# Kernel tuning notes

Measured on AMD Instinct MI355X. Metric: run time of the kernel, lower is better.

Reference implementation:

```python
import jax, jax.numpy as jnp
import numpy as np
import math

EMBED_SIZE = 2048
HEADS = 32
GROUPS = 8
HEAD_DIM = EMBED_SIZE // HEADS          # 64
HPG = HEADS // GROUPS                   # heads per group = 4
N, L = 4, 1024


def setup_inputs() -> dict:
    key = jax.random.key(0)
    k1, k2, k3, k4, k5 = jax.random.split(key, 5)
    values = jax.random.normal(k1, (N, L, EMBED_SIZE), dtype=jnp.float32)
    keys = jax.random.normal(k2, (N, L, EMBED_SIZE), dtype=jnp.float32)
    queries = jax.random.normal(k3, (N, L, EMBED_SIZE), dtype=jnp.float32)
    mask = jnp.ones((N, 1, 1, L, L), dtype=jnp.int32)
    # fc_out: Linear(heads*head_dim -> embed_size), torch default init ~ U(-1/sqrt(in), 1/sqrt(in))
    bound = 1.0 / math.sqrt(EMBED_SIZE)
    W_out = jax.random.uniform(k4, (EMBED_SIZE, EMBED_SIZE), jnp.float32, -bound, bound)
    b_out = jax.random.uniform(k5, (EMBED_SIZE,), jnp.float32, -bound, bound)
    return {"values": values, "keys": keys, "queries": queries, "mask": mask,
            "W_out": W_out, "b_out": b_out}


def reference(values, keys, queries, mask, W_out, b_out):
    n, q_len, _ = queries.shape
    k_len = keys.shape[1]
    # split into (N, L, groups, heads_per_group, head_dim)
    v = values.reshape(n, k_len, GROUPS, HPG, HEAD_DIM)
    k = keys.reshape(n, k_len, GROUPS, HPG, HEAD_DIM)
    q = queries.reshape(n, q_len, GROUPS, HPG, HEAD_DIM)
    # scores: (N, groups, heads_per_group, q, k)
    energy = jnp.einsum('nqghd,nkghd->nghqk', q, k)
    energy = jnp.where(mask == 0, jnp.float32(-1e20), energy)
    attn = jax.nn.softmax(energy / jnp.sqrt(jnp.float32(EMBED_SIZE)), axis=-1)
    out = jnp.einsum('nghqk,nkghd->nqghd', attn, v).reshape(n, q_len, EMBED_SIZE)
    return out @ W_out.T + b_out
```

## Files before the change

kernel.cpp:

```cpp
#include <hip/hip_runtime.h>
#include <math.h>


#define LSEQ 1024
#define EMB  2048

typedef __bf16 bf16x8 __attribute__((ext_vector_type(8)));
typedef __bf16 bf16x4 __attribute__((ext_vector_type(4)));
typedef float floatx4 __attribute__((ext_vector_type(4)));
typedef unsigned short ushort8v __attribute__((ext_vector_type(8)));

__device__ __forceinline__ float4 ld4(const float* p) { return *(const float4*)p; }

__device__ __forceinline__ unsigned short f2bf(float x) {
    unsigned u = __float_as_uint(x);
    u += 0x7FFFu + ((u >> 16) & 1u);
    return (unsigned short)(u >> 16);
}

__device__ __forceinline__ void gl_lds16(const void* g, void* l) {
    __builtin_amdgcn_global_load_lds((const __attribute__((address_space(1))) void*)g,
                                     (__attribute__((address_space(3))) void*)l, 16, 0, 0);
}

__device__ __forceinline__ void stage64(const unsigned short* g, size_t gstride,
                                        unsigned short* lds) {
    const int t = threadIdx.x;
    #pragma unroll
    for (int h = 0; h < 2; h++) {
        const int idx = h * 256 + t;
        const int r   = idx >> 3;
        const int sl  = (idx & 7) ^ (r & 7);
        gl_lds16(g + (size_t)r * gstride + sl * 8, lds + idx * 8);
    }
}

__device__ __forceinline__ void stage128(const unsigned short* g, size_t gstride,
                                         unsigned short* lds) {
    const int t = threadIdx.x;
    #pragma unroll
    for (int h = 0; h < 4; h++) {
        const int idx = h * 256 + t;
        const int r   = idx >> 3;
        const int sl  = (idx & 7) ^ (r & 7);
        gl_lds16(g + (size_t)r * gstride + sl * 8, lds + idx * 8);
    }
}

__device__ __forceinline__ bf16x8 frag_ld(const unsigned short* lds, int row, int seg) {
    return *(const bf16x8*)(lds + row * 64 + ((seg ^ (row & 7)) * 8));
}

__global__ __launch_bounds__(256)
void prep_all(const float* __restrict__ K, unsigned short* __restrict__ Kh,
              const float* __restrict__ W, unsigned short* __restrict__ Wh,
              const float* __restrict__ V, unsigned short* __restrict__ Vt) {
    __shared__ float tile[64][69];
    const int bid = blockIdx.x;
    const int t = threadIdx.x;
    if (bid < 4096) {
        const size_t i = ((size_t)bid * 256 + t) * 8;
        float4 a = ld4(K + i), b = ld4(K + i + 4);
        ushort8v h;
        h[0] = f2bf(a.x); h[1] = f2bf(a.y); h[2] = f2bf(a.z); h[3] = f2bf(a.w);
        h[4] = f2bf(b.x); h[5] = f2bf(b.y); h[6] = f2bf(b.z); h[7] = f2bf(b.w);
        *(ushort8v*)(Kh + i) = h;
    } else if (bid < 6144) {
        const size_t i = ((size_t)(bid - 4096) * 256 + t) * 8;
        float4 a = ld4(W + i), b = ld4(W + i + 4);
        ushort8v h;
        h[0] = f2bf(a.x); h[1] = f2bf(a.y); h[2] = f2bf(a.z); h[3] = f2bf(a.w);
        h[4] = f2bf(b.x); h[5] = f2bf(b.y); h[6] = f2bf(b.z); h[7] = f2bf(b.w);
        *(ushort8v*)(Wh + i) = h;
    } else {
        const int vb = bid - 6144;
        const int kc = vb & 15, h = (vb >> 4) & 31, n = vb >> 9;
        {
            const int rr = t >> 2, c4 = (t & 3) * 16;
            const float* src = V + ((size_t)(n * LSEQ + kc * 64 + rr)) * EMB + h * 64 + c4;
            #pragma unroll
            for (int j = 0; j < 4; j++)
                *(float4*)&tile[rr][c4 + j * 4] = ld4(src + j * 4);
        }
        __syncthreads();
        const int d = t >> 2, k16 = (t & 3) * 16;
        unsigned short* dst = Vt + ((size_t)((n * 32 + h) * 64 + d)) * 1024 + kc * 64 + k16;
        ushort8v o0, o1;
        #pragma unroll
        for (int j = 0; j < 8; j++) o0[j] = f2bf(tile[k16 + j][d]);
        #pragma unroll
        for (int j = 0; j < 8; j++) o1[j] = f2bf(tile[k16 + 8 + j][d]);
        *(ushort8v*)dst = o0;
        *(ushort8v*)(dst + 8) = o1;
    }
}

#define PSTR 76
__global__ __launch_bounds__(256, 4)
void gqa_attn_mfma(const float* __restrict__ Qf, const unsigned short* __restrict__ Kh,
                   const unsigned short* __restrict__ Vt, unsigned short* __restrict__ Ah) {
    __shared__ unsigned short sK[64 * 64];
    __shared__ unsigned short sV[64 * 64];
    __shared__ unsigned short sQP[128 * PSTR];

    const int bid  = blockIdx.x;
    const int hl   = bid & 127;
    const int qt   = bid >> 7;
    const int head = hl & 31;
    const int n    = hl >> 5;
    const int q0   = qt * 128;

    const int t = threadIdx.x, w = t >> 6, lane = t & 63;
    const int lm = lane & 15, cq = lane >> 4;
    const int w32 = w * 32;

    const float scale2 = 0.03187936190857805f;

    const unsigned short* Kb = Kh + ((size_t)(n * LSEQ)) * EMB + head * 64;
    const unsigned short* Vb = Vt + ((size_t)(n * 32 + head)) * 64 * 1024;

    stage64(Kb, EMB, sK);
    stage64(Vb, 1024, sV);

    #pragma unroll
    for (int h = 0; h < 4; h++) {
        const int idx = h * 256 + t;
        const int r = idx >> 3;
        const int sl = idx & 7;
        const int sp = sl ^ (r & 7);
        const float* src = Qf + ((size_t)(n * LSEQ + q0 + r)) * EMB + head * 64 + sl * 8;
        float4 x0 = ld4(src), x1 = ld4(src + 4);
        float xs[8] = {x0.x, x0.y, x0.z, x0.w, x1.x, x1.y, x1.z, x1.w};
        ushort8v hv;
        #pragma unroll
        for (int j = 0; j < 8; j++) hv[j] = f2bf(xs[j] * scale2);
        *(ushort8v*)(sQP + r * 64 + sp * 8) = hv;
    }
    __syncthreads();

    bf16x8 qf[2][2];
    #pragma unroll
    for (int set = 0; set < 2; set++)
        #pragma unroll
        for (int hf = 0; hf < 2; hf++)
            qf[set][hf] = frag_ld(sQP, w32 + set * 16 + lm, hf * 4 + cq);
    __syncthreads();

    unsigned short* sP = sQP;

    floatx4 o[2][4];
    #pragma unroll
    for (int set = 0; set < 2; set++)
        #pragma unroll
        for (int dt = 0; dt < 4; dt++) o[set][dt] = (floatx4){0.f, 0.f, 0.f, 0.f};
    float lpart[2] = {0.f, 0.f};

    for (int kc = 0; kc < 16; kc++) {
        floatx4 s[2][4];
        #pragma unroll
        for (int set = 0; set < 2; set++)
            #pragma unroll
            for (int kt = 0; kt < 4; kt++) s[set][kt] = (floatx4){0.f, 0.f, 0.f, 0.f};
        #pragma unroll
        for (int kt = 0; kt < 4; kt++) {
            #pragma unroll
            for (int hf = 0; hf < 2; hf++) {
                bf16x8 kf = frag_ld(sK, kt * 16 + lm, hf * 4 + cq);
                s[0][kt] = __builtin_amdgcn_mfma_f32_16x16x32_bf16(kf, qf[0][hf], s[0][kt], 0, 0, 0);
                s[1][kt] = __builtin_amdgcn_mfma_f32_16x16x32_bf16(kf, qf[1][hf], s[1][kt], 0, 0, 0);
            }
        }

        #pragma unroll
        for (int set = 0; set < 2; set++) {
            #pragma unroll
            for (int kt = 0; kt < 4; kt++) {
                float p[4];
                #pragma unroll
                for (int r = 0; r < 4; r++) {
                    p[r] = __builtin_amdgcn_exp2f(s[set][kt][r]);
                    lpart[set] += p[r];
                }
                bf16x4 pk;
                #pragma unroll
                for (int r = 0; r < 4; r++) pk[r] = (__bf16)p[r];
                *(bf16x4*)(sP + (w32 + set * 16 + lm) * PSTR + kt * 16 + cq * 4) = pk;
            }
        }

        #pragma unroll
        for (int hf = 0; hf < 2; hf++) {
            bf16x8 pf0 = *(const bf16x8*)(sP + (w32 + lm) * PSTR + hf * 32 + cq * 8);
            bf16x8 pf1 = *(const bf16x8*)(sP + (w32 + 16 + lm) * PSTR + hf * 32 + cq * 8);
            #pragma unroll
            for (int dt = 0; dt < 4; dt++) {
                bf16x8 vf = frag_ld(sV, dt * 16 + lm, hf * 4 + cq);
                o[0][dt] = __builtin_amdgcn_mfma_f32_16x16x32_bf16(pf0, vf, o[0][dt], 0, 0, 0);
                o[1][dt] = __builtin_amdgcn_mfma_f32_16x16x32_bf16(pf1, vf, o[1][dt], 0, 0, 0);
            }
        }

        if (kc < 15) {
            __syncthreads();
            stage64(Kb + (size_t)((kc + 1) * 64) * EMB, EMB, sK);
            stage64(Vb + (kc + 1) * 64, 1024, sV);
            __syncthreads();
        }
    }

    #pragma unroll
    for (int set = 0; set < 2; set++) {
        float lred = lpart[set];
        lred += __shfl_xor(lred, 16);
        lred += __shfl_xor(lred, 32);
        const size_t obase =
            ((size_t)(n * LSEQ + q0 + w32 + set * 16 + cq * 4)) * EMB + head * 64 + lm;
        #pragma unroll
        for (int r = 0; r < 4; r++) {
            const float inv = 1.f / __shfl(lred, cq * 4 + r);
            #pragma unroll
            for (int dt = 0; dt < 4; dt++)
                Ah[obase + (size_t)r * EMB + dt * 16] = f2bf(o[set][dt][r] * inv);
        }
    }
}

__global__ __launch_bounds__(256, 2)
void out_proj_bf16(const unsigned short* __restrict__ A, const unsigned short* __restrict__ B,
                   const float* __restrict__ bias, float* __restrict__ C) {
    __shared__ unsigned short sA[128 * 64];
    __shared__ unsigned short sB[128 * 64];

    const int t = threadIdx.x, bid = blockIdx.x;
    const int nb = bid & 15, mb = bid >> 4;
    const int m0 = mb * 128, n0 = nb * 128;
    const int wave = t >> 6, lane = t & 63;
    const int wr = wave >> 1, wc = wave & 1;
    const int lm = lane & 15, cq = lane >> 4;

    floatx4 acc[4][4];
    #pragma unroll
    for (int i = 0; i < 4; i++)
        #pragma unroll
        for (int j = 0; j < 4; j++)
            acc[i][j] = (floatx4){0.f, 0.f, 0.f, 0.f};

    for (int kc = 0; kc < 32; kc++) {
        __syncthreads();
        stage128(A + (size_t)m0 * 2048 + kc * 64, 2048, sA);
        stage128(B + (size_t)n0 * 2048 + kc * 64, 2048, sB);
        __syncthreads();

        bf16x8 af[4][2], bf[4][2];
        #pragma unroll
        for (int i = 0; i < 4; i++)
            #pragma unroll
            for (int kk = 0; kk < 2; kk++)
                af[i][kk] = frag_ld(sA, wr * 64 + i * 16 + lm, kk * 4 + cq);
        #pragma unroll
        for (int j = 0; j < 4; j++)
            #pragma unroll
            for (int kk = 0; kk < 2; kk++)
                bf[j][kk] = frag_ld(sB, wc * 64 + j * 16 + lm, kk * 4 + cq);
        #pragma unroll
        for (int i = 0; i < 4; i++)
            #pragma unroll
            for (int j = 0; j < 4; j++)
                #pragma unroll
                for (int kk = 0; kk < 2; kk++)
                    acc[i][j] = __builtin_amdgcn_mfma_f32_16x16x32_bf16(af[i][kk], bf[j][kk],
                                                                        acc[i][j], 0, 0, 0);
    }

    const int lr = cq * 4;
    #pragma unroll
    for (int j = 0; j < 4; j++) {
        const int col = n0 + wc * 64 + j * 16 + lm;
        const float bv = bias[col];
        #pragma unroll
        for (int i = 0; i < 4; i++) {
            const int rowb = m0 + wr * 64 + i * 16 + lr;
            #pragma unroll
            for (int r = 0; r < 4; r++)
                C[(size_t)(rowb + r) * 2048 + col] = acc[i][j][r] + bv;
        }
    }
}

extern "C" void kernel_launch(void* const* d_in, const int* in_sizes, int n_in,
                              void* d_out, int out_size, void* d_ws, size_t ws_size,
                              hipStream_t stream) {
    const float* V = (const float*)d_in[0];
    const float* K = (const float*)d_in[1];
    const float* Q = (const float*)d_in[2];
    const float* W = (const float*)d_in[4];
    const float* b = (const float*)d_in[5];
    float* out = (float*)d_out;

    unsigned short* Ah = (unsigned short*)d_ws;
    unsigned short* Kh = Ah + (size_t)4096 * 2048;
    unsigned short* Vt = Kh + (size_t)4096 * 2048;
    unsigned short* Wh = Vt + (size_t)4 * 32 * 64 * 1024;

    prep_all<<<8192, 256, 0, stream>>>(K, Kh, W, Wh, V, Vt);
    gqa_attn_mfma<<<1024, 256, 0, stream>>>(Q, Kh, Vt, Ah);
    out_proj_bf16<<<512, 256, 0, stream>>>(Ah, Wh, b, out);
}
```

Measured before the change: 257.1 us.

## Load K/V/Q MFMA fragments directly from global memory, dropping LDS staging

The attention kernel stops staging K and V tiles into shared memory each iteration and drops the per-iteration block barriers. Each wave now loads its K and V MFMA fragments straight from global memory (relying on L2/L1 reuse across the four waves), and Q fragments are loaded and converted in registers. Only the P tile stays in shared memory, which shrinks LDS use, and launch bounds are lowered to 3 blocks per CU. The risk is that every wave re-reads the same K/V data from cache, and global load latency is exposed with no explicit prefetch.

```diff
diff --git a/kernel.cpp b/kernel.cpp
--- a/kernel.cpp
+++ b/kernel.cpp
@@ -96,12 +96,10 @@
 }
 
 #define PSTR 76
-__global__ __launch_bounds__(256, 4)
+__global__ __launch_bounds__(256, 3)
 void gqa_attn_mfma(const float* __restrict__ Qf, const unsigned short* __restrict__ Kh,
                    const unsigned short* __restrict__ Vt, unsigned short* __restrict__ Ah) {
-    __shared__ unsigned short sK[64 * 64];
-    __shared__ unsigned short sV[64 * 64];
-    __shared__ unsigned short sQP[128 * PSTR];
+    __shared__ unsigned short sP[128 * PSTR];
 
     const int bid  = blockIdx.x;
     const int hl   = bid & 127;
@@ -119,34 +117,22 @@
     const unsigned short* Kb = Kh + ((size_t)(n * LSEQ)) * EMB + head * 64;
     const unsigned short* Vb = Vt + ((size_t)(n * 32 + head)) * 64 * 1024;
 
-    stage64(Kb, EMB, sK);
-    stage64(Vb, 1024, sV);
-
-    #pragma unroll
-    for (int h = 0; h < 4; h++) {
-        const int idx = h * 256 + t;
-        const int r = idx >> 3;
-        const int sl = idx & 7;
-        const int sp = sl ^ (r & 7);
-        const float* src = Qf + ((size_t)(n * LSEQ + q0 + r)) * EMB + head * 64 + sl * 8;
-        float4 x0 = ld4(src), x1 = ld4(src + 4);
-        float xs[8] = {x0.x, x0.y, x0.z, x0.w, x1.x, x1.y, x1.z, x1.w};
-        ushort8v hv;
-        #pragma unroll
-        for (int j = 0; j < 8; j++) hv[j] = f2bf(xs[j] * scale2);
-        *(ushort8v*)(sQP + r * 64 + sp * 8) = hv;
-    }
-    __syncthreads();
-
     bf16x8 qf[2][2];
     #pragma unroll
-    for (int set = 0; set < 2; set++)
-        #pragma unroll
-        for (int hf = 0; hf < 2; hf++)
-            qf[set][hf] = frag_ld(sQP, w32 + set * 16 + lm, hf * 4 + cq);
-    __syncthreads();
-
-    unsigned short* sP = sQP;
+    for (int set = 0; set < 2; set++) {
+        const float* qrow = Qf + ((size_t)(n * LSEQ + q0 + w32 + set * 16 + lm)) * EMB + head * 64;
+        #pragma unroll
+        for (int hf = 0; hf < 2; hf++) {
+            const float* src = qrow + (hf * 4 + cq) * 8;
+            float4 a = ld4(src), b = ld4(src + 4);
+            bf16x8 q;
+            q[0] = (__bf16)(a.x * scale2); q[1] = (__bf16)(a.y * scale2);
+            q[2] = (__bf16)(a.z * scale2); q[3] = (__bf16)(a.w * scale2);
+            q[4] = (__bf16)(b.x * scale2); q[5] = (__bf16)(b.y * scale2);
+            q[6] = (__bf16)(b.z * scale2); q[7] = (__bf16)(b.w * scale2);
+            qf[set][hf] = q;
+        }
+    }
 
     floatx4 o[2][4];
     #pragma unroll
@@ -155,7 +141,21 @@
         for (int dt = 0; dt < 4; dt++) o[set][dt] = (floatx4){0.f, 0.f, 0.f, 0.f};
     float lpart[2] = {0.f, 0.f};
 
+    const int kseg = (lane >> 4) * 8;
+
     for (int kc = 0; kc < 16; kc++) {
+        const unsigned short* Kt = Kb + (size_t)(kc * 64) * EMB;
+        const unsigned short* Vk = Vb + kc * 64;
+
+        bf16x8 kf[4][2];
+        #pragma unroll
+        for (int kt = 0; kt < 4; kt++) {
+            const unsigned short* krow = Kt + (size_t)(kt * 16 + lm) * EMB;
+            #pragma unroll
+            for (int hf = 0; hf < 2; hf++)
+                kf[kt][hf] = *(const bf16x8*)(krow + (hf * 4 + cq) * 8);
+        }
+
         floatx4 s[2][4];
         #pragma unroll
         for (int set = 0; set < 2; set++)
@@ -165,9 +165,8 @@
         for (int kt = 0; kt < 4; kt++) {
             #pragma unroll
             for (int hf = 0; hf < 2; hf++) {
-                bf16x8 kf = frag_ld(sK, kt * 16 + lm, hf * 4 + cq);
-                s[0][kt] = __builtin_amdgcn_mfma_f32_16x16x32_bf16(kf, qf[0][hf], s[0][kt], 0, 0, 0);
-                s[1][kt] = __builtin_amdgcn_mfma_f32_16x16x32_bf16(kf, qf[1][hf], s[1][kt], 0, 0, 0);
+                s[0][kt] = __builtin_amdgcn_mfma_f32_16x16x32_bf16(kf[kt][hf], qf[0][hf], s[0][kt], 0, 0, 0);
+                s[1][kt] = __builtin_amdgcn_mfma_f32_16x16x32_bf16(kf[kt][hf], qf[1][hf], s[1][kt], 0, 0, 0);
             }
         }
 
@@ -188,25 +187,27 @@
             }
         }
 
+        bf16x8 vf[4][2];
+        #pragma unroll
+        for (int dt = 0; dt < 4; dt++) {
+            const unsigned short* vrow = Vk + (dt * 16 + lm) * 1024;
+            #pragma unroll
+            for (int hf = 0; hf < 2; hf++)
+                vf[dt][hf] = *(const bf16x8*)(vrow + (hf * 4 + cq) * 8);
+        }
+
         #pragma unroll
         for (int hf = 0; hf < 2; hf++) {
             bf16x8 pf0 = *(const bf16x8*)(sP + (w32 + lm) * PSTR + hf * 32 + cq * 8);
             bf16x8 pf1 = *(const bf16x8*)(sP + (w32 + 16 + lm) * PSTR + hf * 32 + cq * 8);
             #pragma unroll
             for (int dt = 0; dt < 4; dt++) {
-                bf16x8 vf = frag_ld(sV, dt * 16 + lm, hf * 4 + cq);
-                o[0][dt] = __builtin_amdgcn_mfma_f32_16x16x32_bf16(pf0, vf, o[0][dt], 0, 0, 0);
-                o[1][dt] = __builtin_amdgcn_mfma_f32_16x16x32_bf16(pf1, vf, o[1][dt], 0, 0, 0);
+                o[0][dt] = __builtin_amdgcn_mfma_f32_16x16x32_bf16(pf0, vf[dt][hf], o[0][dt], 0, 0, 0);
+                o[1][dt] = __builtin_amdgcn_mfma_f32_16x16x32_bf16(pf1, vf[dt][hf], o[1][dt], 0, 0, 0);
             }
         }
-
-        if (kc < 15) {
-            __syncthreads();
-            stage64(Kb + (size_t)((kc + 1) * 64) * EMB, EMB, sK);
-            stage64(Vb + (kc + 1) * 64, 1024, sV);
-            __syncthreads();
-        }
-    }
+    }
+    (void)kseg;
 
     #pragma unroll
     for (int set = 0; set < 2; set++) {
```

Measured after the change: 315.7 us. 1.23x slower.

## Double-buffer K/V tiles in LDS to overlap staging with attention compute

Applied to the files above, without the earlier changes.

The attention kernel now uses two LDS buffers for the K/V tiles. It stages the next 64-key chunk into one buffer while computing on the other, and the loop is unrolled by two through an ATTN_STEP macro. This halves the barriers per chunk and is meant to hide global-to-LDS load latency behind the MFMA and exp work. In exchange, LDS use per block grows and the launch-bounds occupancy hint drops from 4 to 3 blocks per CU, which may reduce latency hiding across waves.

```diff
diff --git a/kernel.cpp b/kernel.cpp
--- a/kernel.cpp
+++ b/kernel.cpp
@@ -96,12 +96,62 @@
 }
 
 #define PSTR 76
-__global__ __launch_bounds__(256, 4)
+
+#define ATTN_STEP(SK, SV)                                                                  \
+    do {                                                                                   \
+        floatx4 s[2][4];                                                                   \
+        _Pragma("unroll")                                                                  \
+        for (int set = 0; set < 2; set++)                                                  \
+            _Pragma("unroll")                                                              \
+            for (int kt = 0; kt < 4; kt++) s[set][kt] = (floatx4){0.f, 0.f, 0.f, 0.f};     \
+        _Pragma("unroll")                                                                  \
+        for (int kt = 0; kt < 4; kt++) {                                                   \
+            _Pragma("unroll")                                                              \
+            for (int hf = 0; hf < 2; hf++) {                                               \
+                bf16x8 kf = frag_ld((SK), kt * 16 + lm, hf * 4 + cq);                      \
+                s[0][kt] = __builtin_amdgcn_mfma_f32_16x16x32_bf16(kf, qf[0][hf],          \
+                                                                   s[0][kt], 0, 0, 0);     \
+                s[1][kt] = __builtin_amdgcn_mfma_f32_16x16x32_bf16(kf, qf[1][hf],          \
+                                                                   s[1][kt], 0, 0, 0);     \
+            }                                                                              \
+        }                                                                                  \
+        _Pragma("unroll")                                                                  \
+        for (int set = 0; set < 2; set++) {                                                \
+            _Pragma("unroll")                                                              \
+            for (int kt = 0; kt < 4; kt++) {                                               \
+                float p[4];                                                                \
+                _Pragma("unroll")                                                          \
+                for (int r = 0; r < 4; r++) {                                              \
+                    p[r] = __builtin_amdgcn_exp2f(s[set][kt][r]);                          \
+                    lpart[set] += p[r];                                                    \
+                }                                                                          \
+                bf16x4 pk;                                                                 \
+                _Pragma("unroll")                                                          \
+                for (int r = 0; r < 4; r++) pk[r] = (__bf16)p[r];                          \
+                *(bf16x4*)(sP + (w32 + set * 16 + lm) * PSTR + kt * 16 + cq * 4) = pk;     \
+            }                                                                              \
+        }                                                                                  \
+        _Pragma("unroll")                                                                  \
+        for (int hf = 0; hf < 2; hf++) {                                                   \
+            bf16x8 pf0 = *(const bf16x8*)(sP + (w32 + lm) * PSTR + hf * 32 + cq * 8);      \
+            bf16x8 pf1 = *(const bf16x8*)(sP + (w32 + 16 + lm) * PSTR + hf * 32 + cq * 8); \
+            _Pragma("unroll")                                                              \
+            for (int dt = 0; dt < 4; dt++) {                                               \
+                bf16x8 vf = frag_ld((SV), dt * 16 + lm, hf * 4 + cq);                      \
+                o[0][dt] = __builtin_amdgcn_mfma_f32_16x16x32_bf16(pf0, vf,                \
+                                                                   o[0][dt], 0, 0, 0);     \
+                o[1][dt] = __builtin_amdgcn_mfma_f32_16x16x32_bf16(pf1, vf,                \
+                                                                   o[1][dt], 0, 0, 0);     \
+            }                                                                              \
+        }                                                                                  \
+    } while (0)
+
+__global__ __launch_bounds__(256, 3)
 void gqa_attn_mfma(const float* __restrict__ Qf, const unsigned short* __restrict__ Kh,
                    const unsigned short* __restrict__ Vt, unsigned short* __restrict__ Ah) {
-    __shared__ unsigned short sK[64 * 64];
-    __shared__ unsigned short sV[64 * 64];
-    __shared__ unsigned short sQP[128 * PSTR];
+    __shared__ unsigned short sA0[8192];
+    __shared__ unsigned short sA1[8192];
+    __shared__ unsigned short sP[128 * PSTR];
 
     const int bid  = blockIdx.x;
     const int hl   = bid & 127;
@@ -119,8 +169,8 @@
     const unsigned short* Kb = Kh + ((size_t)(n * LSEQ)) * EMB + head * 64;
     const unsigned short* Vb = Vt + ((size_t)(n * 32 + head)) * 64 * 1024;
 
-    stage64(Kb, EMB, sK);
-    stage64(Vb, 1024, sV);
+    stage64(Kb, EMB, sA0);
+    stage64(Vb, 1024, sA0 + 4096);
 
     #pragma unroll
     for (int h = 0; h < 4; h++) {
@@ -134,7 +184,7 @@
         ushort8v hv;
         #pragma unroll
         for (int j = 0; j < 8; j++) hv[j] = f2bf(xs[j] * scale2);
-        *(ushort8v*)(sQP + r * 64 + sp * 8) = hv;
+        *(ushort8v*)(sA1 + r * 64 + sp * 8) = hv;
     }
     __syncthreads();
 
@@ -143,10 +193,8 @@
     for (int set = 0; set < 2; set++)
         #pragma unroll
         for (int hf = 0; hf < 2; hf++)
-            qf[set][hf] = frag_ld(sQP, w32 + set * 16 + lm, hf * 4 + cq);
+            qf[set][hf] = frag_ld(sA1, w32 + set * 16 + lm, hf * 4 + cq);
     __syncthreads();
-
-    unsigned short* sP = sQP;
 
     floatx4 o[2][4];
     #pragma unroll
@@ -155,57 +203,19 @@
         for (int dt = 0; dt < 4; dt++) o[set][dt] = (floatx4){0.f, 0.f, 0.f, 0.f};
     float lpart[2] = {0.f, 0.f};
 
-    for (int kc = 0; kc < 16; kc++) {
-        floatx4 s[2][4];
-        #pragma unroll
-        for (int set = 0; set < 2; set++)
-            #pragma unroll
-            for (int kt = 0; kt < 4; kt++) s[set][kt] = (floatx4){0.f, 0.f, 0.f, 0.f};
-        #pragma unroll
-        for (int kt = 0; kt < 4; kt++) {
-            #pragma unroll
-            for (int hf = 0; hf < 2; hf++) {
-                bf16x8 kf = frag_ld(sK, kt * 16 + lm, hf * 4 + cq);
-                s[0][kt] = __builtin_amdgcn_mfma_f32_16x16x32_bf16(kf, qf[0][hf], s[0][kt], 0, 0, 0);
-                s[1][kt] = __builtin_amdgcn_mfma_f32_16x16x32_bf16(kf, qf[1][hf], s[1][kt], 0, 0, 0);
-            }
+    for (int kb = 0; kb < 8; kb++) {
+        const int kc0 = kb * 2;
+        stage64(Kb + (size_t)((kc0 + 1) * 64) * EMB, EMB, sA1);
+        stage64(Vb + (kc0 + 1) * 64, 1024, sA1 + 4096);
+        ATTN_STEP(sA0, sA0 + 4096);
+        __syncthreads();
+
+        if (kb < 7) {
+            stage64(Kb + (size_t)((kc0 + 2) * 64) * EMB, EMB, sA0);
+            stage64(Vb + (kc0 + 2) * 64, 1024, sA0 + 4096);
         }
-
-        #pragma unroll
-        for (int set = 0; set < 2; set++) {
-            #pragma unroll
-            for (int kt = 0; kt < 4; kt++) {
-                float p[4];
-                #pragma unroll
-                for (int r = 0; r < 4; r++) {
-                    p[r] = __builtin_amdgcn_exp2f(s[set][kt][r]);
-                    lpart[set] += p[r];
-                }
-                bf16x4 pk;
-                #pragma unroll
-                for (int r = 0; r < 4; r++) pk[r] = (__bf16)p[r];
-                *(bf16x4*)(sP + (w32 + set * 16 + lm) * PSTR + kt * 16 + cq * 4) = pk;
-            }
-        }
-
-        #pragma unroll
-        for (int hf = 0; hf < 2; hf++) {
-            bf16x8 pf0 = *(const bf16x8*)(sP + (w32 + lm) * PSTR + hf * 32 + cq * 8);
-            bf16x8 pf1 = *(const bf16x8*)(sP + (w32 + 16 + lm) * PSTR + hf * 32 + cq * 8);
-            #pragma unroll
-            for (int dt = 0; dt < 4; dt++) {
-                bf16x8 vf = frag_ld(sV, dt * 16 + lm, hf * 4 + cq);
-                o[0][dt] = __builtin_amdgcn_mfma_f32_16x16x32_bf16(pf0, vf, o[0][dt], 0, 0, 0);
-                o[1][dt] = __builtin_amdgcn_mfma_f32_16x16x32_bf16(pf1, vf, o[1][dt], 0, 0, 0);
-            }
-        }
-
-        if (kc < 15) {
-            __syncthreads();
-            stage64(Kb + (size_t)((kc + 1) * 64) * EMB, EMB, sK);
-            stage64(Vb + (kc + 1) * 64, 1024, sV);
-            __syncthreads();
-        }
+        ATTN_STEP(sA1, sA1 + 4096);
+        __syncthreads();
     }
 
     #pragma unroll
```

Result: faster. 243.4 us (-5.3%).
